# Kernel optimization log

Measured on AMD Instinct MI355X. Metric: run time of the kernel, lower is better.

## Reference

```python
import jax, jax.numpy as jnp
import numpy as np

N_NODES = 50000
N_EDGES = 600000
N_RELS = 16
N_GRAPHS = 128
IN_DIM = 128
REL_LAYERS = [128, 256, 128]
HIDDEN = [128, 256, 128]
N_CLASSES = 8


def setup_inputs() -> dict:
    key = jax.random.key(0)
    ks = jax.random.split(key, 24)
    inp = {}
    inp["h"] = jax.random.normal(ks[0], (N_NODES, IN_DIM), dtype=jnp.float32)
    inp["src"] = jax.random.randint(ks[1], (N_EDGES,), 0, N_NODES)
    inp["dst"] = jax.random.randint(ks[2], (N_EDGES,), 0, N_NODES)
    inp["rel_types"] = jax.random.randint(ks[3], (N_EDGES,), 0, N_RELS)
    inp["graph_ids"] = jnp.sort(jax.random.randint(ks[4], (N_NODES,), 0, N_GRAPHS))
    # RelGraphConv params per layer: W_rel [R,din,dout], W_loop [din,dout], b [dout]
    prev = IN_DIM
    ki = 5
    for i, d in enumerate(REL_LAYERS):
        inp[f"W_rel{i}"] = jax.random.normal(ks[ki], (N_RELS, prev, d), dtype=jnp.float32) * 0.05
        inp[f"W_loop{i}"] = jax.random.normal(ks[ki + 1], (prev, d), dtype=jnp.float32) * 0.05
        inp[f"b{i}"] = jnp.zeros((d,), dtype=jnp.float32)
        prev = d
        ki += 2
    for i, d in enumerate(HIDDEN):
        inp[f"Wh{i}"] = jax.random.normal(ks[ki], (prev, d), dtype=jnp.float32) * 0.05
        inp[f"bh{i}"] = jnp.zeros((d,), dtype=jnp.float32)
        prev = d
        ki += 1
    inp["Wc"] = jax.random.normal(ks[ki], (prev, N_CLASSES), dtype=jnp.float32) * 0.05
    inp["bc"] = jnp.zeros((N_CLASSES,), dtype=jnp.float32)
    return inp


def _rel_graph_conv(h, src, dst, rel, W_rel, W_loop, b):
    # transform every node under every relation: [R, N, dout]
    t = jnp.einsum("nd,rde->rne", h, W_rel)
    msgs = t[rel, src]  # [E, dout] gather per edge
    agg = jax.ops.segment_sum(msgs, dst, num_segments=h.shape[0])
    return jax.nn.relu(agg + h @ W_loop + b)  # self-loop + bias (DGL defaults)


def _forward(h, src, dst, rel_types, graph_ids,
             W_rel0, W_loop0, b0, W_rel1, W_loop1, b1, W_rel2, W_loop2, b2,
             Wh0, bh0, Wh1, bh1, Wh2, bh2, Wc, bc):
    h = h.astype(jnp.float32)
    for Wr, Wl, b in ((W_rel0, W_loop0, b0), (W_rel1, W_loop1, b1), (W_rel2, W_loop2, b2)):
        h = _rel_graph_conv(h, src, dst, rel_types, Wr, Wl, b)
    # dgl.mean_nodes: per-graph mean pooling
    sums = jax.ops.segment_sum(h, graph_ids, num_segments=N_GRAPHS)
    cnts = jax.ops.segment_sum(jnp.ones((h.shape[0],), h.dtype), graph_ids, num_segments=N_GRAPHS)
    hg = sums / jnp.maximum(cnts, 1.0)[:, None]
    for W, b in ((Wh0, bh0), (Wh1, bh1), (Wh2, bh2)):
        hg = jax.nn.relu(hg @ W + b)
    return jax.nn.softmax(hg @ Wc + bc, axis=1)


def reference(h, src, dst, rel_types, graph_ids,
              W_rel0, W_loop0, b0, W_rel1, W_loop1, b1, W_rel2, W_loop2, b2,
              Wh0, bh0, Wh1, bh1, Wh2, bh2, Wc, bc):
    return _forward(h, src, dst, rel_types, graph_ids,
                    W_rel0, W_loop0, b0, W_rel1, W_loop1, b1, W_rel2, W_loop2, b2,
                    Wh0, bh0, Wh1, bh1, Wh2, bh2, Wc, bc)
```

## Files before the change

### kernel.cpp

```cpp
#include <hip/hip_runtime.h>
#include <stdint.h>

#define NN 50000
#define NE 600000
#define NR 16
#define NG 128
#define TS 128
#define SCAN_B 512
#define NB_SCAN ((NN + SCAN_B - 1) / SCAN_B)
#define MAXB 1024

typedef short bf16x8 __attribute__((ext_vector_type(8)));
typedef float f32x4 __attribute__((ext_vector_type(4)));

static __device__ __forceinline__ unsigned short f2bf(float x) {
    unsigned int b = __float_as_uint(x);
    b += 0x7FFFu + ((b >> 16) & 1u);
    return (unsigned short)(b >> 16);
}
static __device__ __forceinline__ float bf2f(unsigned short u) {
    return __uint_as_float(((unsigned int)u) << 16);
}


__global__ void k_zero(int* bcnt, int* cursor, int* ncnt, int* ncur, float* hg, float* gcnt) {
    int i = blockIdx.x * 256 + threadIdx.x;
    if (i < MAXB) { bcnt[i] = 0; cursor[i] = 0; }
    if (i < NN) { ncnt[i] = 0; ncur[i] = 0; }
    if (i < NG * 128) hg[i] = 0.f;
    if (i < NG) gcnt[i] = 0.f;
}

__global__ void k_hist(const int* __restrict__ rel, const int* __restrict__ dst,
                       int* __restrict__ bcnt, int* __restrict__ ncnt, int npc, int B) {
    __shared__ int lh[MAXB];
    for (int i = threadIdx.x; i < B; i += 256) lh[i] = 0;
    __syncthreads();
    for (int e = blockIdx.x * blockDim.x + threadIdx.x; e < NE; e += gridDim.x * blockDim.x) {
        int d = dst[e];
        atomicAdd(&lh[(d / npc) * NR + rel[e]], 1);
        atomicAdd(&ncnt[d], 1);
    }
    __syncthreads();
    for (int i = threadIdx.x; i < B; i += 256) atomicAdd(&bcnt[i], lh[i]);
}

__global__ void k_scan1(const int* __restrict__ ncnt, int* __restrict__ bsum) {
    __shared__ int s[SCAN_B];
    int i = blockIdx.x * SCAN_B + threadIdx.x;
    s[threadIdx.x] = (i < NN) ? ncnt[i] : 0;
    __syncthreads();
    for (int off = SCAN_B / 2; off > 0; off >>= 1) {
        if (threadIdx.x < off) s[threadIdx.x] += s[threadIdx.x + off];
        __syncthreads();
    }
    if (threadIdx.x == 0) bsum[blockIdx.x] = s[0];
}

__global__ void k_scan2(const int* __restrict__ bsum, int* __restrict__ bpref, int* __restrict__ rowptr) {
    if (threadIdx.x == 0 && blockIdx.x == 0) {
        int run = 0;
        for (int b = 0; b < NB_SCAN; ++b) { bpref[b] = run; run += bsum[b]; }
        rowptr[NN] = run;
    }
}

__global__ void k_scan3(const int* __restrict__ ncnt, const int* __restrict__ bpref,
                        int* __restrict__ rowptr) {
    __shared__ int s[SCAN_B];
    int i = blockIdx.x * SCAN_B + threadIdx.x;
    int val = (i < NN) ? ncnt[i] : 0;
    s[threadIdx.x] = val;
    __syncthreads();
    for (int off = 1; off < SCAN_B; off <<= 1) {
        int x = (threadIdx.x >= off) ? s[threadIdx.x - off] : 0;
        __syncthreads();
        s[threadIdx.x] += x;
        __syncthreads();
    }
    if (i < NN) rowptr[i] = bpref[blockIdx.x] + s[threadIdx.x] - val;
}

__global__ __launch_bounds__(1024)
void k_scan_buckets(const int* __restrict__ bcnt, int B, int npc,
                    const int* __restrict__ rowptr,
                    int* __restrict__ boff, int* __restrict__ tstart,
                    int4* __restrict__ tilemap) {
    __shared__ int s1[MAXB], s2[MAXB];
    __shared__ int e_ex[MAXB + 1], t_ex[MAXB + 1];
    int tid = threadIdx.x;
    int v1 = (tid < B) ? bcnt[tid] : 0;
    int v2 = (v1 + TS - 1) / TS;
    s1[tid] = v1; s2[tid] = v2;
    __syncthreads();
    for (int off = 1; off < MAXB; off <<= 1) {
        int a1 = (tid >= off) ? s1[tid - off] : 0;
        int a2 = (tid >= off) ? s2[tid - off] : 0;
        __syncthreads();
        s1[tid] += a1; s2[tid] += a2;
        __syncthreads();
    }
    if (tid < B) {
        e_ex[tid] = s1[tid] - v1;
        t_ex[tid] = s2[tid] - v2;
        boff[tid] = e_ex[tid];
        tstart[tid] = t_ex[tid];
        if (tid == B - 1) {
            e_ex[B] = s1[tid]; t_ex[B] = s2[tid];
            boff[B] = s1[tid]; tstart[B] = s2[tid];
        }
    }
    __syncthreads();
    int T = t_ex[B];
    for (int t = tid; t < T; t += 1024) {
        int lo = 0, hi = B - 1;
        while (lo < hi) {
            int mid = (lo + hi + 1) >> 1;
            if (t_ex[mid] <= t) lo = mid; else hi = mid - 1;
        }
        int b = lo;
        int tt = t - t_ex[b];
        int v1b = e_ex[b + 1] - e_ex[b];
        int rem = v1b - tt * TS;
        int cnt = rem < TS ? rem : TS;
        int chunk = b >> 4;
        int nstart = chunk * npc; if (nstart > NN) nstart = NN;
        tilemap[t] = make_int4(b & (NR - 1), e_ex[b] + tt * TS, cnt, rowptr[nstart]);
    }
}

__global__ void k_scatter(const int* __restrict__ rel, const int* __restrict__ dst,
                          const int* __restrict__ src,
                          const int* __restrict__ boff, int* __restrict__ cursor,
                          const int* __restrict__ rowptr, int* __restrict__ ncur,
                          int* __restrict__ srcs, int* __restrict__ dpos, int npc, int B) {
    __shared__ int lh[MAXB];
    const int CH = 4096;
    int e0 = blockIdx.x * CH;
    for (int i = threadIdx.x; i < B; i += 256) lh[i] = 0;
    __syncthreads();
    for (int i = threadIdx.x; i < CH; i += 256) {
        int e = e0 + i;
        if (e < NE) atomicAdd(&lh[(dst[e] / npc) * NR + rel[e]], 1);
    }
    __syncthreads();
    for (int i = threadIdx.x; i < B; i += 256) {
        int c = lh[i];
        lh[i] = (c > 0) ? atomicAdd(&cursor[i], c) : 0;
    }
    __syncthreads();
    for (int i = threadIdx.x; i < CH; i += 256) {
        int e = e0 + i;
        if (e < NE) {
            int d = dst[e];
            int b = (d / npc) * NR + rel[e];
            int p = boff[b] + atomicAdd(&lh[b], 1);
            int pd = rowptr[d] + atomicAdd(&ncur[d], 1);
            srcs[p] = src[e];
            dpos[p] = pd;
        }
    }
}


__global__ void k_hconv(const float* __restrict__ h, unsigned short* __restrict__ hb, int n4) {
    int i = blockIdx.x * 256 + threadIdx.x;
    if (i < n4) {
        float4 v = reinterpret_cast<const float4*>(h)[i];
        ushort4 o = { f2bf(v.x), f2bf(v.y), f2bf(v.z), f2bf(v.w) };
        reinterpret_cast<ushort4*>(hb)[i] = o;
    }
}

__global__ void k_wconv_all(const float* Wr0, const float* Wr1, const float* Wr2,
                            const float* Wl0, const float* Wl1, const float* Wl2,
                            unsigned short* Wt0, unsigned short* Wt1, unsigned short* Wt2,
                            unsigned short* Wlt0, unsigned short* Wlt1, unsigned short* Wlt2) {
    const float* W; unsigned short* O; int R, Kd, Nd;
    switch (blockIdx.y) {
        case 0:  W = Wr0; O = Wt0;  R = NR; Kd = 128; Nd = 128; break;
        case 1:  W = Wr1; O = Wt1;  R = NR; Kd = 128; Nd = 256; break;
        case 2:  W = Wr2; O = Wt2;  R = NR; Kd = 256; Nd = 128; break;
        case 3:  W = Wl0; O = Wlt0; R = 1;  Kd = 128; Nd = 128; break;
        case 4:  W = Wl1; O = Wlt1; R = 1;  Kd = 128; Nd = 256; break;
        default: W = Wl2; O = Wlt2; R = 1;  Kd = 256; Nd = 128; break;
    }
    int total = R * Kd * Nd;
    for (int i = blockIdx.x * 256 + threadIdx.x; i < total; i += gridDim.x * 256) {
        int r = i / (Kd * Nd);
        int rem = i - r * Kd * Nd;
        int k = rem / Nd;
        int n = rem - k * Nd;
        O[((size_t)r * Nd + n) * Kd + k] = f2bf(W[i]);
    }
}


template<int K>
__global__ __launch_bounds__(256, 4)
void k_dense_mfma(const unsigned short* __restrict__ hb,
                  const unsigned short* __restrict__ Wlt,
                  const float* __restrict__ bias,
                  float* __restrict__ outbuf, int ldn) {
    __shared__ __align__(16) unsigned short As[128][72];
    __shared__ __align__(16) unsigned short Bs[128][72];
    const int tid = threadIdx.x;
    const int row0 = blockIdx.x * 128;
    const int colbase = blockIdx.y * 128;
    const int lane = tid & 63, w = tid >> 6;
    const int quad = lane >> 4, col = lane & 15;
    const int srow = tid >> 3, sk = (tid & 7) * 8;

    f32x4 acc[8][2];
#pragma unroll
    for (int i = 0; i < 8; ++i) { acc[i][0] = 0.f; acc[i][1] = 0.f; }

    for (int k0 = 0; k0 < K; k0 += 64) {
        __syncthreads();
#pragma unroll
        for (int pp = 0; pp < 4; ++pp) {
            int rw = pp * 32 + srow;
            int ar = row0 + rw; if (ar >= NN) ar = NN - 1;
            *reinterpret_cast<uint4*>(&As[rw][sk]) =
                *reinterpret_cast<const uint4*>(hb + (size_t)ar * K + k0 + sk);
            *reinterpret_cast<uint4*>(&Bs[rw][sk]) =
                *reinterpret_cast<const uint4*>(Wlt + (size_t)(colbase + rw) * K + k0 + sk);
        }
        __syncthreads();
#pragma unroll
        for (int s = 0; s < 2; ++s) {
            bf16x8 bf0 = *reinterpret_cast<const bf16x8*>(&Bs[w * 32 + col][s * 32 + quad * 8]);
            bf16x8 bf1 = *reinterpret_cast<const bf16x8*>(&Bs[w * 32 + 16 + col][s * 32 + quad * 8]);
#pragma unroll
            for (int rt = 0; rt < 8; ++rt) {
                bf16x8 af = *reinterpret_cast<const bf16x8*>(&As[rt * 16 + col][s * 32 + quad * 8]);
                acc[rt][0] = __builtin_amdgcn_mfma_f32_16x16x32_bf16(af, bf0, acc[rt][0], 0, 0, 0);
                acc[rt][1] = __builtin_amdgcn_mfma_f32_16x16x32_bf16(af, bf1, acc[rt][1], 0, 0, 0);
            }
        }
    }
    float bv0 = bias[colbase + w * 32 + col];
    float bv1 = bias[colbase + w * 32 + 16 + col];
#pragma unroll
    for (int rt = 0; rt < 8; ++rt) {
#pragma unroll
        for (int reg = 0; reg < 4; ++reg) {
            int r = row0 + rt * 16 + quad * 4 + reg;
            if (r < NN) {
                float* dp = outbuf + (size_t)r * ldn + colbase + w * 32;
                dp[col] = acc[rt][0][reg] + bv0;
                dp[16 + col] = acc[rt][1][reg] + bv1;
            }
        }
    }
}


template<int K>
__global__ __launch_bounds__(256, 4)
void k_edge_mfma(const unsigned short* __restrict__ hb,
                 const unsigned short* __restrict__ Wt,
                 int ldn, int colbase,
                 const int* __restrict__ srcs, const int* __restrict__ dpos,
                 const int4* __restrict__ tilemap, const int* __restrict__ tstart,
                 int chunkBase,
                 unsigned short* __restrict__ msg, int capRows) {
    const int tb0 = tstart[chunkBase];
    const int tend = tstart[chunkBase + NR];
    const int t = tb0 + blockIdx.x;
    if (t >= tend) return;
    const int4 tm = tilemap[t];
    const int r = tm.x, e0 = tm.y, cnt = tm.z, cES = tm.w;

    __shared__ __align__(16) unsigned short As[128][136];
    __shared__ int s_src[TS], s_out[TS];
    const int tid = threadIdx.x;
    if (tid < TS) {
        int ei = e0 + (tid < cnt ? tid : cnt - 1);
        s_src[tid] = srcs[ei];
        int row = dpos[ei] - cES;
        s_out[tid] = (tid < cnt && row < capRows) ? row : -1;
    }
    __syncthreads();

    const unsigned short* Wb = Wt + ((size_t)r * ldn + colbase) * K;
    const int lane = tid & 63, w = tid >> 6;
    const int quad = lane >> 4, col = lane & 15;
    const int asr = tid >> 4, ask = (tid & 15) * 8;

    f32x4 acc[8][2];
#pragma unroll
    for (int i = 0; i < 8; ++i) { acc[i][0] = 0.f; acc[i][1] = 0.f; }

    for (int kk = 0; kk < K; kk += 128) {
        if (kk) __syncthreads();
#pragma unroll
        for (int q = 0; q < 8; ++q) {
            int rw = q * 16 + asr;
            *reinterpret_cast<uint4*>(&As[rw][ask]) =
                *reinterpret_cast<const uint4*>(hb + (size_t)s_src[rw] * K + kk + ask);
        }
        __syncthreads();
#pragma unroll
        for (int k32 = 0; k32 < 4; ++k32) {
            bf16x8 bf0 = *reinterpret_cast<const bf16x8*>(
                Wb + (size_t)(w * 32 + col) * K + kk + k32 * 32 + quad * 8);
            bf16x8 bf1 = *reinterpret_cast<const bf16x8*>(
                Wb + (size_t)(w * 32 + 16 + col) * K + kk + k32 * 32 + quad * 8);
#pragma unroll
            for (int rt = 0; rt < 8; ++rt) {
                bf16x8 af = *reinterpret_cast<const bf16x8*>(&As[rt * 16 + col][k32 * 32 + quad * 8]);
                acc[rt][0] = __builtin_amdgcn_mfma_f32_16x16x32_bf16(af, bf0, acc[rt][0], 0, 0, 0);
                acc[rt][1] = __builtin_amdgcn_mfma_f32_16x16x32_bf16(af, bf1, acc[rt][1], 0, 0, 0);
            }
        }
    }
#pragma unroll
    for (int rt = 0; rt < 8; ++rt) {
#pragma unroll
        for (int reg = 0; reg < 4; ++reg) {
            int m = rt * 16 + quad * 4 + reg;
            int o = s_out[m];
            if (o >= 0) {
                unsigned short* dp = msg + (size_t)o * 128 + w * 32;
                dp[col] = f2bf(acc[rt][0][reg]);
                dp[16 + col] = f2bf(acc[rt][1][reg]);
            }
        }
    }
}

__global__ __launch_bounds__(256)
void k_reduce(const unsigned short* __restrict__ msg,
              const float* __restrict__ selfb, int ld_self, int co_self,
              unsigned short* __restrict__ out_bf, int ld_bf, int co_bf,
              float* __restrict__ out_f32, int ld_f32, int co_f32,
              const int* __restrict__ rowptr, int n0, int npc, int capRows) {
    int idx = blockIdx.x * 4 + (threadIdx.x >> 6);
    int n = n0 + idx;
    if (idx >= npc || n >= NN) return;
    int lane = threadIdx.x & 63;
    int cES = rowptr[n0];
    float2 acc = *reinterpret_cast<const float2*>(selfb + (size_t)n * ld_self + co_self + lane * 2);
    int j0 = rowptr[n], j1 = rowptr[n + 1];
    for (int j = j0; j < j1; ++j) {
        int rr = j - cES;
        if (rr >= capRows) break;
        unsigned int m = *reinterpret_cast<const unsigned int*>(msg + (size_t)rr * 128 + lane * 2);
        acc.x += bf2f((unsigned short)(m & 0xffffu));
        acc.y += bf2f((unsigned short)(m >> 16));
    }
    acc.x = acc.x > 0.f ? acc.x : 0.f;
    acc.y = acc.y > 0.f ? acc.y : 0.f;
    if (out_bf) {
        unsigned int o = (unsigned int)f2bf(acc.x) | ((unsigned int)f2bf(acc.y) << 16);
        *reinterpret_cast<unsigned int*>(out_bf + (size_t)n * ld_bf + co_bf + lane * 2) = o;
    }
    if (out_f32) {
        *reinterpret_cast<float2*>(out_f32 + (size_t)n * ld_f32 + co_f32 + lane * 2) = acc;
    }
}


__global__ void k_pool(const float* __restrict__ h, const int* __restrict__ gid,
                       float* __restrict__ hg, float* __restrict__ gcnt) {
    const int c = threadIdx.x;
    int n0 = blockIdx.x * 64;
    if (n0 >= NN) return;
    int end = n0 + 64; if (end > NN) end = NN;
    int cur = gid[n0];
    float run = 0.f, crun = 0.f;
    for (int n = n0; n < end; ++n) {
        int g = gid[n];
        if (g != cur) {
            atomicAdd(&hg[cur * 128 + c], run);
            if (c == 0) atomicAdd(&gcnt[cur], crun);
            run = 0.f; crun = 0.f; cur = g;
        }
        run += h[(size_t)n * 128 + c];
        crun += 1.f;
    }
    atomicAdd(&hg[cur * 128 + c], run);
    if (c == 0) atomicAdd(&gcnt[cur], crun);
}

__global__ __launch_bounds__(256)
void k_head(const float* __restrict__ hg, const float* __restrict__ gcnt,
            const float* __restrict__ Wh0, const float* __restrict__ bh0,
            const float* __restrict__ Wh1, const float* __restrict__ bh1,
            const float* __restrict__ Wh2, const float* __restrict__ bh2,
            const float* __restrict__ Wc, const float* __restrict__ bc,
            float* __restrict__ out) {
    __shared__ float x0[128], x1[128], x2[256], x3[128], sl[8];
    int g = blockIdx.x, t = threadIdx.x;
    if (t < 128) {
        float c = gcnt[g];
        x0[t] = hg[g * 128 + t] / (c > 1.f ? c : 1.f);
    }
    __syncthreads();
    if (t < 128) {
        float a = bh0[t];
        for (int k = 0; k < 128; ++k) a += x0[k] * Wh0[k * 128 + t];
        x1[t] = a > 0.f ? a : 0.f;
    }
    __syncthreads();
    {
        float a = bh1[t];
        for (int k = 0; k < 128; ++k) a += x1[k] * Wh1[k * 256 + t];
        x2[t] = a > 0.f ? a : 0.f;
    }
    __syncthreads();
    if (t < 128) {
        float a = bh2[t];
        for (int k = 0; k < 256; ++k) a += x2[k] * Wh2[k * 128 + t];
        x3[t] = a > 0.f ? a : 0.f;
    }
    __syncthreads();
    if (t < 8) {
        float a = bc[t];
        for (int k = 0; k < 128; ++k) a += x3[k] * Wc[k * 8 + t];
        sl[t] = a;
    }
    __syncthreads();
    if (t == 0) {
        float m = sl[0];
        for (int c = 1; c < 8; ++c) m = sl[c] > m ? sl[c] : m;
        float s = 0.f, e[8];
        for (int c = 0; c < 8; ++c) { e[c] = expf(sl[c] - m); s += e[c]; }
        for (int c = 0; c < 8; ++c) out[g * 8 + c] = e[c] / s;
    }
}


extern "C" void kernel_launch(void* const* d_in, const int* in_sizes, int n_in,
                              void* d_out, int out_size, void* d_ws, size_t ws_size,
                              hipStream_t stream) {
    const float* h0   = (const float*)d_in[0];
    const int* src    = (const int*)d_in[1];
    const int* dst    = (const int*)d_in[2];
    const int* rel    = (const int*)d_in[3];
    const int* gid    = (const int*)d_in[4];
    const float* Wr0  = (const float*)d_in[5];
    const float* Wl0  = (const float*)d_in[6];
    const float* b0   = (const float*)d_in[7];
    const float* Wr1  = (const float*)d_in[8];
    const float* Wl1  = (const float*)d_in[9];
    const float* b1   = (const float*)d_in[10];
    const float* Wr2  = (const float*)d_in[11];
    const float* Wl2  = (const float*)d_in[12];
    const float* b2   = (const float*)d_in[13];
    const float* Wh0  = (const float*)d_in[14];
    const float* bh0  = (const float*)d_in[15];
    const float* Wh1  = (const float*)d_in[16];
    const float* bh1  = (const float*)d_in[17];
    const float* Wh2  = (const float*)d_in[18];
    const float* bh2  = (const float*)d_in[19];
    const float* Wc   = (const float*)d_in[20];
    const float* bc   = (const float*)d_in[21];
    float* out = (float*)d_out;

    char* p = (char*)d_ws;
    auto alloc = [&](size_t bytes) { char* q = p; p += (bytes + 255) & ~(size_t)255; return q; };
    float* bufS  = (float*)alloc((size_t)NN * 256 * 4);
    unsigned short* hbA = (unsigned short*)alloc((size_t)NN * 256 * 2);
    unsigned short* hbB = (unsigned short*)alloc((size_t)NN * 128 * 2);
    unsigned short* Wt0 = (unsigned short*)alloc((size_t)NR * 128 * 128 * 2);
    unsigned short* Wt1 = (unsigned short*)alloc((size_t)NR * 256 * 128 * 2);
    unsigned short* Wt2 = (unsigned short*)alloc((size_t)NR * 128 * 256 * 2);
    unsigned short* Wlt0 = (unsigned short*)alloc((size_t)128 * 128 * 2);
    unsigned short* Wlt1 = (unsigned short*)alloc((size_t)256 * 128 * 2);
    unsigned short* Wlt2 = (unsigned short*)alloc((size_t)128 * 256 * 2);
    int* srcs    = (int*)alloc((size_t)NE * 4);
    int* dpos    = (int*)alloc((size_t)NE * 4);
    int* ncnt    = (int*)alloc((size_t)NN * 4);
    int* ncur    = (int*)alloc((size_t)NN * 4);
    int* rowptr  = (int*)alloc((size_t)(NN + 1) * 4);
    int* bsum    = (int*)alloc(NB_SCAN * 4);
    int* bpref   = (int*)alloc(NB_SCAN * 4);
    int* bcnt    = (int*)alloc(MAXB * 4);
    int* boff    = (int*)alloc((MAXB + 1) * 4);
    int* tstart  = (int*)alloc((MAXB + 1) * 4);
    int* cursor  = (int*)alloc(MAXB * 4);
    int4* tilemap = (int4*)alloc((size_t)(NE / TS + MAXB + 64) * 16);
    float* hg    = (float*)alloc((size_t)NG * 128 * 4);
    float* gcnt  = (float*)alloc(NG * 4);
    unsigned short* msg = (unsigned short*)p;

    long long avail = (long long)ws_size - (long long)(p - (char*)d_ws);
    if (avail < (1 << 20)) avail = (1 << 20);
    long long capR64 = avail / 256;
    int C = 64;
    for (int c = 1; c <= 64; ++c) {
        double need = (double)NE / c * 1.15 + 4096.0;
        if ((double)capR64 >= need) { C = c; break; }
    }
    int npc = (NN + C - 1) / C;
    int B = C * NR;
    int capRows = capR64 > 2000000000LL ? 2000000000 : (int)capR64;
    int TPC = (int)((double)NE / C * 1.15 / TS) + NR + 8;
    int RDB = (npc + 3) / 4;

    k_zero<<<(NN + 255) / 256, 256, 0, stream>>>(bcnt, cursor, ncnt, ncur, hg, gcnt);
    k_hist<<<256, 256, 0, stream>>>(rel, dst, bcnt, ncnt, npc, B);
    k_scan1<<<NB_SCAN, SCAN_B, 0, stream>>>(ncnt, bsum);
    k_scan2<<<1, 64, 0, stream>>>(bsum, bpref, rowptr);
    k_scan3<<<NB_SCAN, SCAN_B, 0, stream>>>(ncnt, bpref, rowptr);
    k_scan_buckets<<<1, MAXB, 0, stream>>>(bcnt, B, npc, rowptr, boff, tstart, tilemap);
    k_scatter<<<(NE + 4095) / 4096, 256, 0, stream>>>(rel, dst, src, boff, cursor, rowptr, ncur, srcs, dpos, npc, B);

    k_hconv<<<(NN * 128 / 4 + 255) / 256, 256, 0, stream>>>(h0, hbA, NN * 128 / 4);
    k_wconv_all<<<dim3(512, 6), 256, 0, stream>>>(Wr0, Wr1, Wr2, Wl0, Wl1, Wl2,
                                                  Wt0, Wt1, Wt2, Wlt0, Wlt1, Wlt2);

    const int RB = (NN + TS - 1) / TS;

    k_dense_mfma<128><<<dim3(RB, 1), 256, 0, stream>>>(hbA, Wlt0, b0, bufS, 128);
    for (int c = 0; c < C; ++c) {
        k_edge_mfma<128><<<TPC, 256, 0, stream>>>(hbA, Wt0, 128, 0, srcs, dpos, tilemap, tstart, c * NR, msg, capRows);
        k_reduce<<<RDB, 256, 0, stream>>>(msg, bufS, 128, 0, hbB, 128, 0, (float*)nullptr, 0, 0, rowptr, c * npc, npc, capRows);
    }

    k_dense_mfma<128><<<dim3(RB, 2), 256, 0, stream>>>(hbB, Wlt1, b1, bufS, 256);
    for (int half = 0; half < 2; ++half) {
        for (int c = 0; c < C; ++c) {
            k_edge_mfma<128><<<TPC, 256, 0, stream>>>(hbB, Wt1, 256, half * 128, srcs, dpos, tilemap, tstart, c * NR, msg, capRows);
            k_reduce<<<RDB, 256, 0, stream>>>(msg, bufS, 256, half * 128, hbA, 256, half * 128, (float*)nullptr, 0, 0, rowptr, c * npc, npc, capRows);
        }
    }

    k_dense_mfma<256><<<dim3(RB, 1), 256, 0, stream>>>(hbA, Wlt2, b2, bufS, 128);
    for (int c = 0; c < C; ++c) {
        k_edge_mfma<256><<<TPC, 256, 0, stream>>>(hbA, Wt2, 128, 0, srcs, dpos, tilemap, tstart, c * NR, msg, capRows);
        k_reduce<<<RDB, 256, 0, stream>>>(msg, bufS, 128, 0, (unsigned short*)nullptr, 0, 0, bufS, 128, 0, rowptr, c * npc, npc, capRows);
    }

    k_pool<<<(NN + 63) / 64, 128, 0, stream>>>(bufS, gid, hg, gcnt);
    k_head<<<NG, 256, 0, stream>>>(hg, gcnt, Wh0, bh0, Wh1, bh1, Wh2, bh2, Wc, bc, out);
}
```

Before: 829.4 us.

## Double-buffer edge gather tiles in LDS and replace zero kernel with memset

The edge MFMA kernel now stages the gathered source rows in 64-wide K chunks across two LDS buffers. The global loads for the next chunk are issued before the MFMAs on the current chunk, so gather latency overlaps compute and LDS use drops. Separately, the counters and accumulators that need zeroing are laid out contiguously and cleared with one hipMemsetAsync instead of a custom kernel. The cost is more register pressure for the prefetched values and one barrier per 64-wide chunk instead of per 128.

```diff
diff --git a/kernel.cpp b/kernel.cpp
--- a/kernel.cpp
+++ b/kernel.cpp
@@ -22,14 +22,6 @@
     return __uint_as_float(((unsigned int)u) << 16);
 }
 
-
-__global__ void k_zero(int* bcnt, int* cursor, int* ncnt, int* ncur, float* hg, float* gcnt) {
-    int i = blockIdx.x * 256 + threadIdx.x;
-    if (i < MAXB) { bcnt[i] = 0; cursor[i] = 0; }
-    if (i < NN) { ncnt[i] = 0; ncur[i] = 0; }
-    if (i < NG * 128) hg[i] = 0.f;
-    if (i < NG) gcnt[i] = 0.f;
-}
 
 __global__ void k_hist(const int* __restrict__ rel, const int* __restrict__ dst,
                        int* __restrict__ bcnt, int* __restrict__ ncnt, int npc, int B) {
@@ -272,7 +264,7 @@
     const int4 tm = tilemap[t];
     const int r = tm.x, e0 = tm.y, cnt = tm.z, cES = tm.w;
 
-    __shared__ __align__(16) unsigned short As[128][136];
+    __shared__ __align__(16) unsigned short As[2][128][72];
     __shared__ int s_src[TS], s_out[TS];
     const int tid = threadIdx.x;
     if (tid < TS) {
@@ -286,34 +278,54 @@
     const unsigned short* Wb = Wt + ((size_t)r * ldn + colbase) * K;
     const int lane = tid & 63, w = tid >> 6;
     const int quad = lane >> 4, col = lane & 15;
-    const int asr = tid >> 4, ask = (tid & 15) * 8;
+    const int srow = tid >> 3, sk = (tid & 7) * 8;
+
+    int myrow[4];
+#pragma unroll
+    for (int q = 0; q < 4; ++q) myrow[q] = s_src[q * 32 + srow];
 
     f32x4 acc[8][2];
 #pragma unroll
     for (int i = 0; i < 8; ++i) { acc[i][0] = 0.f; acc[i][1] = 0.f; }
 
-    for (int kk = 0; kk < K; kk += 128) {
-        if (kk) __syncthreads();
-#pragma unroll
-        for (int q = 0; q < 8; ++q) {
-            int rw = q * 16 + asr;
-            *reinterpret_cast<uint4*>(&As[rw][ask]) =
-                *reinterpret_cast<const uint4*>(hb + (size_t)s_src[rw] * K + kk + ask);
-        }
-        __syncthreads();
-#pragma unroll
-        for (int k32 = 0; k32 < 4; ++k32) {
+    const int NCH = K / 64;
+    {
+        uint4 v[4];
+#pragma unroll
+        for (int q = 0; q < 4; ++q)
+            v[q] = *reinterpret_cast<const uint4*>(hb + (size_t)myrow[q] * K + sk);
+#pragma unroll
+        for (int q = 0; q < 4; ++q)
+            *reinterpret_cast<uint4*>(&As[0][q * 32 + srow][sk]) = v[q];
+    }
+    __syncthreads();
+#pragma unroll
+    for (int c = 0; c < NCH; ++c) {
+        uint4 v[4];
+        if (c + 1 < NCH) {
+#pragma unroll
+            for (int q = 0; q < 4; ++q)
+                v[q] = *reinterpret_cast<const uint4*>(hb + (size_t)myrow[q] * K + (c + 1) * 64 + sk);
+        }
+#pragma unroll
+        for (int k32 = 0; k32 < 2; ++k32) {
             bf16x8 bf0 = *reinterpret_cast<const bf16x8*>(
-                Wb + (size_t)(w * 32 + col) * K + kk + k32 * 32 + quad * 8);
+                Wb + (size_t)(w * 32 + col) * K + c * 64 + k32 * 32 + quad * 8);
             bf16x8 bf1 = *reinterpret_cast<const bf16x8*>(
-                Wb + (size_t)(w * 32 + 16 + col) * K + kk + k32 * 32 + quad * 8);
+                Wb + (size_t)(w * 32 + 16 + col) * K + c * 64 + k32 * 32 + quad * 8);
 #pragma unroll
             for (int rt = 0; rt < 8; ++rt) {
-                bf16x8 af = *reinterpret_cast<const bf16x8*>(&As[rt * 16 + col][k32 * 32 + quad * 8]);
+                bf16x8 af = *reinterpret_cast<const bf16x8*>(&As[c & 1][rt * 16 + col][k32 * 32 + quad * 8]);
                 acc[rt][0] = __builtin_amdgcn_mfma_f32_16x16x32_bf16(af, bf0, acc[rt][0], 0, 0, 0);
                 acc[rt][1] = __builtin_amdgcn_mfma_f32_16x16x32_bf16(af, bf1, acc[rt][1], 0, 0, 0);
             }
         }
+        if (c + 1 < NCH) {
+#pragma unroll
+            for (int q = 0; q < 4; ++q)
+                *reinterpret_cast<uint4*>(&As[(c + 1) & 1][q * 32 + srow][sk]) = v[q];
+        }
+        __syncthreads();
     }
 #pragma unroll
     for (int rt = 0; rt < 8; ++rt) {
@@ -472,18 +484,20 @@
     unsigned short* Wlt2 = (unsigned short*)alloc((size_t)128 * 256 * 2);
     int* srcs    = (int*)alloc((size_t)NE * 4);
     int* dpos    = (int*)alloc((size_t)NE * 4);
-    int* ncnt    = (int*)alloc((size_t)NN * 4);
-    int* ncur    = (int*)alloc((size_t)NN * 4);
     int* rowptr  = (int*)alloc((size_t)(NN + 1) * 4);
     int* bsum    = (int*)alloc(NB_SCAN * 4);
     int* bpref   = (int*)alloc(NB_SCAN * 4);
-    int* bcnt    = (int*)alloc(MAXB * 4);
     int* boff    = (int*)alloc((MAXB + 1) * 4);
     int* tstart  = (int*)alloc((MAXB + 1) * 4);
+    int4* tilemap = (int4*)alloc((size_t)(NE / TS + MAXB + 64) * 16);
+    char* zbase  = p;
+    int* bcnt    = (int*)alloc(MAXB * 4);
     int* cursor  = (int*)alloc(MAXB * 4);
-    int4* tilemap = (int4*)alloc((size_t)(NE / TS + MAXB + 64) * 16);
+    int* ncnt    = (int*)alloc((size_t)NN * 4);
+    int* ncur    = (int*)alloc((size_t)NN * 4);
     float* hg    = (float*)alloc((size_t)NG * 128 * 4);
     float* gcnt  = (float*)alloc(NG * 4);
+    size_t zlen  = (size_t)(p - zbase);
     unsigned short* msg = (unsigned short*)p;
 
     long long avail = (long long)ws_size - (long long)(p - (char*)d_ws);
@@ -500,7 +514,7 @@
     int TPC = (int)((double)NE / C * 1.15 / TS) + NR + 8;
     int RDB = (npc + 3) / 4;
 
-    k_zero<<<(NN + 255) / 256, 256, 0, stream>>>(bcnt, cursor, ncnt, ncur, hg, gcnt);
+    hipMemsetAsync(zbase, 0, zlen, stream);
     k_hist<<<256, 256, 0, stream>>>(rel, dst, bcnt, ncnt, npc, B);
     k_scan1<<<NB_SCAN, SCAN_B, 0, stream>>>(ncnt, bsum);
     k_scan2<<<1, 64, 0, stream>>>(bsum, bpref, rowptr);
```

Result: no change. 815.7 us (-1.7%).
